# Kernel optimization log

Hardware: AMD Instinct MI355X
Metric: run time of the kernel (lower is better)

## Reference

```python
import jax, jax.numpy as jnp
import numpy as np

NEG_SLOPE = 0.2  # PyG GATv2Conv default negative_slope


def gatv2_layer(x, src, dst, edge_attr, Wl, bl, Wr, br, We, att, bias, n_nodes):
    """Faithful PyG GATv2Conv (concat=True, eval mode / no dropout).
    x: [N, Fin]; src/dst: [E]; edge_attr: [E, Fe]; att: [H, C].
    Returns [N, H*C].
    """
    H, C = att.shape
    xl = (x @ Wl + bl).reshape(-1, H, C)        # source-side transform (x_j)
    xr = (x @ Wr + br).reshape(-1, H, C)        # target-side transform (x_i)
    e_emb = (edge_attr @ We).reshape(-1, H, C)
    # per-edge pre-activation: x_i + x_j + edge
    g = jax.nn.leaky_relu(xl[src] + xr[dst] + e_emb, NEG_SLOPE)  # [E, H, C]
    logits = jnp.einsum('ehc,hc->eh', g, att)                    # [E, H]
    # segment softmax grouped by destination node
    m = jax.ops.segment_max(logits, dst, num_segments=n_nodes)   # [N, H]
    m = jnp.where(jnp.isfinite(m), m, 0.0)                       # empty segments
    a = jnp.exp(logits - m[dst])
    denom = jax.ops.segment_sum(a, dst, num_segments=n_nodes)    # [N, H]
    alpha = a / (denom[dst] + 1e-16)
    msg = xl[src] * alpha[:, :, None]                            # [E, H, C]
    out = jax.ops.segment_sum(msg, dst, num_segments=n_nodes)    # [N, H, C]
    return out.reshape(n_nodes, H * C) + bias


def setup_inputs() -> dict:
    key = jax.random.key(0)
    ks = jax.random.split(key, 24)
    N, E = 100000, 1600000
    Fin, Hd, Fe = 6, 64, 2
    g = lambda k, shp: (jax.random.normal(k, shp, dtype=jnp.float32) * 0.1)
    inp = {
        'x': jax.random.normal(ks[0], (N, Fin), dtype=jnp.float32),
        'edge_index': jax.random.randint(ks[1], (2, E), 0, N, dtype=jnp.int32),
        'edge_attr': jax.random.normal(ks[2], (E, Fe), dtype=jnp.float32),
        # layer 1: heads=2, out=64 -> H*C = 128
        'Wl1': g(ks[3], (Fin, 128)), 'bl1': jnp.zeros((128,), jnp.float32),
        'Wr1': g(ks[4], (Fin, 128)), 'br1': jnp.zeros((128,), jnp.float32),
        'We1': g(ks[5], (Fe, 128)),
        'att1': g(ks[6], (2, Hd)),
        'bias1': jnp.zeros((128,), jnp.float32),
        # layer 2: heads=1, in=128, out=64
        'Wl2': g(ks[7], (128, Hd)), 'bl2': jnp.zeros((Hd,), jnp.float32),
        'Wr2': g(ks[8], (128, Hd)), 'br2': jnp.zeros((Hd,), jnp.float32),
        'We2': g(ks[9], (Fe, Hd)),
        'att2': g(ks[10], (1, Hd)),
        'bias2': jnp.zeros((Hd,), jnp.float32),
        # MLP head
        'Wh1': g(ks[11], (Hd, Hd)), 'bh1': jnp.zeros((Hd,), jnp.float32),
        'Wh2': g(ks[12], (Hd, 1)), 'bh2': jnp.zeros((1,), jnp.float32),
    }
    return inp


def reference(x, edge_index, edge_attr,
              Wl1, bl1, Wr1, br1, We1, att1, bias1,
              Wl2, bl2, Wr2, br2, We2, att2, bias2,
              Wh1, bh1, Wh2, bh2):
    N = x.shape[0]
    src, dst = edge_index[0], edge_index[1]
    h = gatv2_layer(x, src, dst, edge_attr, Wl1, bl1, Wr1, br1, We1, att1, bias1, N)
    h = jax.nn.relu(h)
    h = gatv2_layer(h, src, dst, edge_attr, Wl2, bl2, Wr2, br2, We2, att2, bias2, N)
    h = jax.nn.relu(h)
    out = jax.nn.relu(h @ Wh1 + bh1) @ Wh2 + bh2  # [N, 1]
    return out[:, 0]
```

## Files before the change

### kernel.cpp

```cpp
#include <hip/hip_runtime.h>
#include <hip/hip_bf16.h>

#define NEG_SLOPE 0.2f
#define LOG2E 1.44269504088896f

#define NB_SHIFT 9
#define NB_NODES 512
#define NBLK_PART 256

typedef _Float16 half8 __attribute__((ext_vector_type(8)));
typedef _Float16 half4 __attribute__((ext_vector_type(4)));
typedef _Float16 half2t __attribute__((ext_vector_type(2)));
typedef float floatx2 __attribute__((ext_vector_type(2)));

__device__ __forceinline__ void ld4(float* d, const float* p) {
    float4 t = *(const float4*)p;
    d[0] = t.x; d[1] = t.y; d[2] = t.z; d[3] = t.w;
}

__device__ __forceinline__ unsigned pack2h(float a, float b) {
    union { half2t h; unsigned u; } pk;
    pk.h[0] = (_Float16)a; pk.h[1] = (_Float16)b;
    return pk.u;
}

__device__ __forceinline__ half2t u2h2(unsigned u) {
    union { unsigned u; half2t h; } c; c.u = u; return c.h;
}
__device__ __forceinline__ half2t f2h2(float a, float b) {
    half2t r; r[0] = (_Float16)a; r[1] = (_Float16)b; return r;
}

#if __has_builtin(__builtin_amdgcn_perm)
#define PERMB(a, b, s) __builtin_amdgcn_perm((a), (b), (s))
#else
__device__ __forceinline__ unsigned PERMB(unsigned a, unsigned b, unsigned s) {
    unsigned long long v = ((unsigned long long)a << 32) | b;
    unsigned r = 0;
#pragma unroll
    for (int i = 0; i < 4; ++i) {
        unsigned idx = (s >> (8 * i)) & 0xFF;
        r |= ((unsigned)(v >> (8 * idx)) & 0xFF) << (8 * i);
    }
    return r;
}
#endif

#if __has_builtin(__builtin_amdgcn_fdot2)
#define FDOT2(a, b, c) __builtin_amdgcn_fdot2((a), (b), (c), false)
#else
#define FDOT2(a, b, c) fmaf((float)(a)[1], (float)(b)[1], fmaf((float)(a)[0], (float)(b)[0], (c)))
#endif

#define DPP_ADD(x, ctrl) \
    ((x) + __int_as_float(__builtin_amdgcn_update_dpp(0, __float_as_int(x), (ctrl), 0xf, 0xf, true)))
#define ROW_REDUCE16(x) do { \
    x = DPP_ADD(x, 0x128); \
    x = DPP_ADD(x, 0x124); \
    x = DPP_ADD(x, 0x122); \
    x = DPP_ADD(x, 0x121); \
} while (0)

#define CHGRP(xl2, xr2, wa, wb, at2, ex, ey, logit) do { \
    half2t z_ = (xl2) + (xr2); \
    z_ = __builtin_elementwise_fma((ex), (wa), z_); \
    z_ = __builtin_elementwise_fma((ey), (wb), z_); \
    z_ = __builtin_elementwise_max(z_, z_ * NEGS); \
    logit = FDOT2(z_, (at2), logit); \
} while (0)

__global__ void __launch_bounds__(256) prep_kernel(
    const float* __restrict__ x,
    const float* __restrict__ Wl1, const float* __restrict__ bl1,
    const float* __restrict__ Wr1, const float* __restrict__ br1,
    _Float16* __restrict__ xlh, _Float16* __restrict__ xrh, int N)
{
    int gt = blockIdx.x * blockDim.x + threadIdx.x;
    int n = gt >> 6, c = gt & 63;
    if (n >= N) return;
    const float* xrow = x + (size_t)n * 6;
    float l0 = bl1[c], l1 = bl1[64 + c];
    float r0 = br1[c], r1 = br1[64 + c];
#pragma unroll
    for (int f = 0; f < 6; ++f) {
        float xv = xrow[f];
        l0 = fmaf(xv, Wl1[f * 128 + c], l0);
        l1 = fmaf(xv, Wl1[f * 128 + 64 + c], l1);
        r0 = fmaf(xv, Wr1[f * 128 + c], r0);
        r1 = fmaf(xv, Wr1[f * 128 + 64 + c], r1);
    }
    *(unsigned*)(xlh + (size_t)n * 128 + 2 * c) = pack2h(l0, l1);
    *(unsigned*)(xrh + (size_t)n * 128 + 2 * c) = pack2h(r0, r1);
}

__global__ void __launch_bounds__(256) partA_count(
    const int* __restrict__ dstv, int* __restrict__ M, int E, int EPB, int NB)
{
    __shared__ int hist[256];
    int blk = blockIdx.x, t = threadIdx.x;
    if (t < NB) hist[t] = 0;
    __syncthreads();
    int s0 = blk * EPB;
    int s1 = min(s0 + EPB, E);
    for (int e = s0 + t; e < s1; e += 256)
        atomicAdd(&hist[((unsigned)dstv[e]) >> NB_SHIFT], 1);
    __syncthreads();
    if (t < NB) M[t * NBLK_PART + blk] = hist[t];
}

__global__ void __launch_bounds__(256) partB1_scanrow(
    int* __restrict__ M, int* __restrict__ btot)
{
    __shared__ int lds[256];
    int bkt = blockIdx.x, t = threadIdx.x;
    int cnt = M[bkt * NBLK_PART + t];
    lds[t] = cnt;
    __syncthreads();
    for (int s = 1; s < 256; s <<= 1) {
        int v = (t >= s) ? lds[t - s] : 0;
        __syncthreads();
        lds[t] += v;
        __syncthreads();
    }
    M[bkt * NBLK_PART + t] = lds[t] - cnt;
    if (t == 255) btot[bkt] = lds[255];
}

__global__ void partB2_scanbkt(const int* __restrict__ btot, int* __restrict__ boff,
                               int* __restrict__ off, int NB, int N, int E)
{
    if (threadIdx.x == 0) {
        int run = 0;
        for (int i = 0; i < NB; ++i) { boff[i] = run; run += btot[i]; }
        boff[NB] = run;
        off[N] = E;
    }
}

__global__ void __launch_bounds__(256) partC_scatter(
    const int* __restrict__ srcv, const int* __restrict__ dstv,
    const float2* __restrict__ ea2, const int* __restrict__ M,
    const int* __restrict__ boff,
    int2* __restrict__ ebuf, int* __restrict__ dbuf,
    int E, int EPB, int NB)
{
    __shared__ int cur[256];
    int blk = blockIdx.x, t = threadIdx.x;
    if (t < NB) cur[t] = M[t * NBLK_PART + blk] + boff[t];
    __syncthreads();
    int s0 = blk * EPB;
    int s1 = min(s0 + EPB, E);
    for (int e = s0 + t; e < s1; e += 256) {
        int d = dstv[e];
        int bkt = ((unsigned)d) >> NB_SHIFT;
        int p = atomicAdd(&cur[bkt], 1);
        float2 ea = ea2[e];
        int2 v; v.x = srcv[e]; v.y = (int)pack2h(ea.x, ea.y);
        ebuf[p] = v;
        dbuf[p] = d;
    }
}

__global__ void __launch_bounds__(256) partD_finalize(
    const int2* __restrict__ ebuf, const int* __restrict__ dbuf,
    const int* __restrict__ boff,
    int* __restrict__ off, int2* __restrict__ csr_edge, int N)
{
    __shared__ int hist[NB_NODES];
    int b = blockIdx.x, t = threadIdx.x;
    int node_base = b << NB_SHIFT;
    int nnodes = min(NB_NODES, N - node_base);
    int seg_s = boff[b], seg_e = boff[b + 1];
    for (int i = t; i < NB_NODES; i += 256) hist[i] = 0;
    __syncthreads();
    for (int e = seg_s + t; e < seg_e; e += 256)
        atomicAdd(&hist[dbuf[e] - node_base], 1);
    __syncthreads();
    if (t == 0) {
        int run = 0;
        for (int i = 0; i < nnodes; ++i) { int c = hist[i]; hist[i] = run; run += c; }
    }
    __syncthreads();
    for (int i = t; i < nnodes; i += 256) off[node_base + i] = seg_s + hist[i];
    __syncthreads();
    for (int e = seg_s + t; e < seg_e; e += 256) {
        int dl = dbuf[e] - node_base;
        int r = atomicAdd(&hist[dl], 1);
        csr_edge[seg_s + r] = ebuf[e];
    }
}

__global__ void __launch_bounds__(256) c1_kernel(
    const int* __restrict__ off, const int2* __restrict__ csr_edge,
    const _Float16* __restrict__ xlh, const _Float16* __restrict__ xrh,
    const float* __restrict__ We1, const float* __restrict__ att1,
    const float* __restrict__ bias1,
    _Float16* __restrict__ h1h, int N)
{
    int wid = (blockIdx.x * blockDim.x + threadIdx.x) >> 6;
    int lane = threadIdx.x & 63;
    if (wid >= N) return;
    int n = wid;
    int g = lane & 15;
    int slot = lane >> 4;
    unsigned gb = (unsigned)(g << 4);

    const half2t NEGS = f2h2(NEG_SLOPE, NEG_SLOPE);

    half2t a0h[2], a1h[2], w00h[2], w01h[2], w10h[2], w11h[2];
    {
        float t[4];
        ld4(t, att1 + 4 * g);
        a0h[0] = f2h2(t[0] * LOG2E, t[1] * LOG2E); a0h[1] = f2h2(t[2] * LOG2E, t[3] * LOG2E);
        ld4(t, att1 + 64 + 4 * g);
        a1h[0] = f2h2(t[0] * LOG2E, t[1] * LOG2E); a1h[1] = f2h2(t[2] * LOG2E, t[3] * LOG2E);
        ld4(t, We1 + 4 * g);        w00h[0] = f2h2(t[0], t[1]); w00h[1] = f2h2(t[2], t[3]);
        ld4(t, We1 + 64 + 4 * g);   w01h[0] = f2h2(t[0], t[1]); w01h[1] = f2h2(t[2], t[3]);
        ld4(t, We1 + 128 + 4 * g);  w10h[0] = f2h2(t[0], t[1]); w10h[1] = f2h2(t[2], t[3]);
        ld4(t, We1 + 192 + 4 * g);  w11h[0] = f2h2(t[0], t[1]); w11h[1] = f2h2(t[2], t[3]);
    }

    half2t xr00, xr01, xr10, xr11;
    {
        half8 xrv = *(const half8*)(xrh + (size_t)n * 128 + 8 * g);
        xr00[0] = xrv[0]; xr00[1] = xrv[2];
        xr01[0] = xrv[4]; xr01[1] = xrv[6];
        xr10[0] = xrv[1]; xr10[1] = xrv[3];
        xr11[0] = xrv[5]; xr11[1] = xrv[7];
    }

    int s = off[n], e = off[n + 1];
    float a0A[4] = {0,0,0,0}, a1A[4] = {0,0,0,0};
    float a0B[4] = {0,0,0,0}, a1B[4] = {0,0,0,0};
    float d0A = 0.f, d1A = 0.f, d0B = 0.f, d1B = 0.f;

    const char* xlb = (const char*)xlh;

    int pA0 = s + slot, pB0 = s + 4 + slot;
    bool vA0 = (pA0 < e), vB0 = (pB0 < e);
    int2 edA0 = csr_edge[vA0 ? pA0 : s];
    int2 edB0 = csr_edge[vB0 ? pB0 : s];
    int pA1 = s + 8 + slot, pB1 = s + 12 + slot;
    bool vA1 = (pA1 < e), vB1 = (pB1 < e);
    int2 edA1 = csr_edge[vA1 ? pA1 : s];
    int2 edB1 = csr_edge[vB1 ? pB1 : s];
    half8 hvA = *(const half8*)(xlb + (((unsigned)edA0.x) << 8) + gb);
    half8 hvB = *(const half8*)(xlb + (((unsigned)edB0.x) << 8) + gb);

    for (int p0 = s; p0 < e; p0 += 8) {
        int pA2 = p0 + 16 + slot, pB2 = p0 + 20 + slot;
        bool vA2 = (pA2 < e), vB2 = (pB2 < e);
        int2 edA2 = csr_edge[vA2 ? pA2 : s];
        int2 edB2 = csr_edge[vB2 ? pB2 : s];

        half8 hvAn = *(const half8*)(xlb + (((unsigned)edA1.x) << 8) + gb);
        half8 hvBn = *(const half8*)(xlb + (((unsigned)edB1.x) << 8) + gb);

        unsigned uA = (unsigned)edA0.y, uB = (unsigned)edB0.y;
        half2t exA = u2h2(PERMB(uA, uA, 0x01000100));
        half2t eyA = u2h2(PERMB(uA, uA, 0x03020302));
        half2t exB = u2h2(PERMB(uB, uB, 0x01000100));
        half2t eyB = u2h2(PERMB(uB, uB, 0x03020302));

        union { half8 h; unsigned u[4]; } HA, HB;
        HA.h = hvA; HB.h = hvB;
        half2t xA00 = u2h2(PERMB(HA.u[1], HA.u[0], 0x05040100));
        half2t xA01 = u2h2(PERMB(HA.u[3], HA.u[2], 0x05040100));
        half2t xA10 = u2h2(PERMB(HA.u[1], HA.u[0], 0x07060302));
        half2t xA11 = u2h2(PERMB(HA.u[3], HA.u[2], 0x07060302));
        half2t xB00 = u2h2(PERMB(HB.u[1], HB.u[0], 0x05040100));
        half2t xB01 = u2h2(PERMB(HB.u[3], HB.u[2], 0x05040100));
        half2t xB10 = u2h2(PERMB(HB.u[1], HB.u[0], 0x07060302));
        half2t xB11 = u2h2(PERMB(HB.u[3], HB.u[2], 0x07060302));

        float pA0f = 0.f, pA1f = 0.f, pB0f = 0.f, pB1f = 0.f;
        CHGRP(xA00, xr00, w00h[0], w10h[0], a0h[0], exA, eyA, pA0f);
        CHGRP(xA01, xr01, w00h[1], w10h[1], a0h[1], exA, eyA, pA0f);
        CHGRP(xA10, xr10, w01h[0], w11h[0], a1h[0], exA, eyA, pA1f);
        CHGRP(xA11, xr11, w01h[1], w11h[1], a1h[1], exA, eyA, pA1f);
        CHGRP(xB00, xr00, w00h[0], w10h[0], a0h[0], exB, eyB, pB0f);
        CHGRP(xB01, xr01, w00h[1], w10h[1], a0h[1], exB, eyB, pB0f);
        CHGRP(xB10, xr10, w01h[0], w11h[0], a1h[0], exB, eyB, pB1f);
        CHGRP(xB11, xr11, w01h[1], w11h[1], a1h[1], exB, eyB, pB1f);

        ROW_REDUCE16(pA0f);
        ROW_REDUCE16(pA1f);
        ROW_REDUCE16(pB0f);
        ROW_REDUCE16(pB1f);

        float eA0 = vA0 ? exp2f(pA0f) : 0.f;
        float eA1 = vA0 ? exp2f(pA1f) : 0.f;
        float eB0 = vB0 ? exp2f(pB0f) : 0.f;
        float eB1 = vB0 ? exp2f(pB1f) : 0.f;
        d0A += eA0; d1A += eA1;
        d0B += eB0; d1B += eB1;

        a0A[0] = fmaf(eA0, (float)hvA[0], a0A[0]);
        a0A[1] = fmaf(eA0, (float)hvA[2], a0A[1]);
        a0A[2] = fmaf(eA0, (float)hvA[4], a0A[2]);
        a0A[3] = fmaf(eA0, (float)hvA[6], a0A[3]);
        a1A[0] = fmaf(eA1, (float)hvA[1], a1A[0]);
        a1A[1] = fmaf(eA1, (float)hvA[3], a1A[1]);
        a1A[2] = fmaf(eA1, (float)hvA[5], a1A[2]);
        a1A[3] = fmaf(eA1, (float)hvA[7], a1A[3]);
        a0B[0] = fmaf(eB0, (float)hvB[0], a0B[0]);
        a0B[1] = fmaf(eB0, (float)hvB[2], a0B[1]);
        a0B[2] = fmaf(eB0, (float)hvB[4], a0B[2]);
        a0B[3] = fmaf(eB0, (float)hvB[6], a0B[3]);
        a1B[0] = fmaf(eB1, (float)hvB[1], a1B[0]);
        a1B[1] = fmaf(eB1, (float)hvB[3], a1B[1]);
        a1B[2] = fmaf(eB1, (float)hvB[5], a1B[2]);
        a1B[3] = fmaf(eB1, (float)hvB[7], a1B[3]);

        edA0 = edA1; edB0 = edB1; vA0 = vA1; vB0 = vB1;
        edA1 = edA2; edB1 = edB2; vA1 = vA2; vB1 = vB2;
        hvA = hvAn; hvB = hvBn;
    }

    float acc0[4], acc1[4];
#pragma unroll
    for (int i = 0; i < 4; ++i) { acc0[i] = a0A[i] + a0B[i]; acc1[i] = a1A[i] + a1B[i]; }
    float d0 = d0A + d0B, d1 = d1A + d1B;
#pragma unroll
    for (int i = 0; i < 4; ++i) {
        acc0[i] += __shfl_xor(acc0[i], 16); acc0[i] += __shfl_xor(acc0[i], 32);
        acc1[i] += __shfl_xor(acc1[i], 16); acc1[i] += __shfl_xor(acc1[i], 32);
    }
    d0 += __shfl_xor(d0, 16); d0 += __shfl_xor(d0, 32);
    d1 += __shfl_xor(d1, 16); d1 += __shfl_xor(d1, 32);

    if (slot == 0) {
        float b0[4], b1[4];
        ld4(b0, bias1 + 4 * g);
        ld4(b1, bias1 + 64 + 4 * g);
        float r0 = 1.f / (d0 + 1e-16f), r1 = 1.f / (d1 + 1e-16f);
        half4 o0, o1;
        o0[0] = (_Float16)fmaxf(fmaf(acc0[0], r0, b0[0]), 0.f);
        o0[1] = (_Float16)fmaxf(fmaf(acc0[1], r0, b0[1]), 0.f);
        o0[2] = (_Float16)fmaxf(fmaf(acc0[2], r0, b0[2]), 0.f);
        o0[3] = (_Float16)fmaxf(fmaf(acc0[3], r0, b0[3]), 0.f);
        o1[0] = (_Float16)fmaxf(fmaf(acc1[0], r1, b1[0]), 0.f);
        o1[1] = (_Float16)fmaxf(fmaf(acc1[1], r1, b1[1]), 0.f);
        o1[2] = (_Float16)fmaxf(fmaf(acc1[2], r1, b1[2]), 0.f);
        o1[3] = (_Float16)fmaxf(fmaf(acc1[3], r1, b1[3]), 0.f);
        *(half4*)(h1h + (size_t)n * 128 + 4 * g) = o0;
        *(half4*)(h1h + (size_t)n * 128 + 64 + 4 * g) = o1;
    }
}

__global__ void __launch_bounds__(256) a2_kernel(
    const _Float16* __restrict__ h1h,
    const float* __restrict__ Wl2, const float* __restrict__ bl2,
    const float* __restrict__ Wr2, const float* __restrict__ br2,
    _Float16* __restrict__ xl2h, _Float16* __restrict__ xr2h, int N)
{
    __shared__ float hs[64 * 128];
    int tid = threadIdx.x;
    int n0 = blockIdx.x * 64;

    for (int i = tid; i < 64 * 16; i += 256) {
        int row = i >> 4;
        int q = i & 15;
        int n = n0 + row;
        float f[8];
        if (n < N) {
            half8 v = *(const half8*)(h1h + (size_t)n * 128 + q * 8);
#pragma unroll
            for (int j = 0; j < 8; ++j) f[j] = (float)v[j];
        } else {
#pragma unroll
            for (int j = 0; j < 8; ++j) f[j] = 0.f;
        }
        *(float4*)(hs + row * 128 + q * 8)     = make_float4(f[0], f[1], f[2], f[3]);
        *(float4*)(hs + row * 128 + q * 8 + 4) = make_float4(f[4], f[5], f[6], f[7]);
    }
    __syncthreads();

    int cslot = tid & 31;
    int jgrp = tid >> 5;
    int c4 = cslot * 4;
    bool isL = (c4 < 64);
    int cc = isL ? c4 : (c4 - 64);
    const float* Wb = (isL ? Wl2 : Wr2) + cc;
    const float* bb = (isL ? bl2 : br2) + cc;
    float4 bias = *(const float4*)bb;

    float acc[8][4];
#pragma unroll
    for (int j = 0; j < 8; ++j) {
        acc[j][0] = bias.x; acc[j][1] = bias.y;
        acc[j][2] = bias.z; acc[j][3] = bias.w;
    }

    const float* hrow = hs + (jgrp * 8) * 128;
#pragma unroll 2
    for (int k4 = 0; k4 < 32; ++k4) {
        float4 w0 = *(const float4*)(Wb + (4 * k4 + 0) * 64);
        float4 w1 = *(const float4*)(Wb + (4 * k4 + 1) * 64);
        float4 w2 = *(const float4*)(Wb + (4 * k4 + 2) * 64);
        float4 w3 = *(const float4*)(Wb + (4 * k4 + 3) * 64);
#pragma unroll
        for (int j = 0; j < 8; ++j) {
            float4 hv = *(const float4*)(hrow + j * 128 + k4 * 4);
            acc[j][0] = fmaf(hv.x, w0.x, acc[j][0]);
            acc[j][1] = fmaf(hv.x, w0.y, acc[j][1]);
            acc[j][2] = fmaf(hv.x, w0.z, acc[j][2]);
            acc[j][3] = fmaf(hv.x, w0.w, acc[j][3]);
            acc[j][0] = fmaf(hv.y, w1.x, acc[j][0]);
            acc[j][1] = fmaf(hv.y, w1.y, acc[j][1]);
            acc[j][2] = fmaf(hv.y, w1.z, acc[j][2]);
            acc[j][3] = fmaf(hv.y, w1.w, acc[j][3]);
            acc[j][0] = fmaf(hv.z, w2.x, acc[j][0]);
            acc[j][1] = fmaf(hv.z, w2.y, acc[j][1]);
            acc[j][2] = fmaf(hv.z, w2.z, acc[j][2]);
            acc[j][3] = fmaf(hv.z, w2.w, acc[j][3]);
            acc[j][0] = fmaf(hv.w, w3.x, acc[j][0]);
            acc[j][1] = fmaf(hv.w, w3.y, acc[j][1]);
            acc[j][2] = fmaf(hv.w, w3.z, acc[j][2]);
            acc[j][3] = fmaf(hv.w, w3.w, acc[j][3]);
        }
    }

    _Float16* outb = isL ? xl2h : xr2h;
#pragma unroll
    for (int j = 0; j < 8; ++j) {
        int n = n0 + jgrp * 8 + j;
        if (n < N) {
            half4 o;
            o[0] = (_Float16)acc[j][0];
            o[1] = (_Float16)acc[j][1];
            o[2] = (_Float16)acc[j][2];
            o[3] = (_Float16)acc[j][3];
            *(half4*)(outb + (size_t)n * 64 + cc) = o;
        }
    }
}

__global__ void __launch_bounds__(256) c2_kernel(
    const int* __restrict__ off, const int2* __restrict__ csr_edge,
    const _Float16* __restrict__ xl2h, const _Float16* __restrict__ xr2h,
    const float* __restrict__ We2, const float* __restrict__ att2,
    const float* __restrict__ bias2,
    float* __restrict__ h2out, int N)
{
    int wid = (blockIdx.x * blockDim.x + threadIdx.x) >> 6;
    int lane = threadIdx.x & 63;
    if (wid >= N) return;
    int n = wid;
    int g = lane & 15;
    int slot = lane >> 4;
    unsigned gb = (unsigned)(g << 3);

    const half2t NEGS = f2h2(NEG_SLOPE, NEG_SLOPE);

    half2t avh[2], w0h[2], w1h[2], xr2[2];
    {
        float t[4];
        ld4(t, att2 + 4 * g);
        avh[0] = f2h2(t[0] * LOG2E, t[1] * LOG2E); avh[1] = f2h2(t[2] * LOG2E, t[3] * LOG2E);
        ld4(t, We2 + 4 * g);       w0h[0] = f2h2(t[0], t[1]); w0h[1] = f2h2(t[2], t[3]);
        ld4(t, We2 + 64 + 4 * g);  w1h[0] = f2h2(t[0], t[1]); w1h[1] = f2h2(t[2], t[3]);
        half4 xh = *(const half4*)(xr2h + (size_t)n * 64 + 4 * g);
        xr2[0][0] = xh[0]; xr2[0][1] = xh[1];
        xr2[1][0] = xh[2]; xr2[1][1] = xh[3];
    }

    int s = off[n], e = off[n + 1];
    float dA = 0.f, dB = 0.f;
    float aA[4] = {0,0,0,0}, aB[4] = {0,0,0,0};

    const char* xlb = (const char*)xl2h;

    int pA0 = s + slot, pB0 = s + 4 + slot;
    bool vA0 = (pA0 < e), vB0 = (pB0 < e);
    int2 edA0 = csr_edge[vA0 ? pA0 : s];
    int2 edB0 = csr_edge[vB0 ? pB0 : s];
    int pA1 = s + 8 + slot, pB1 = s + 12 + slot;
    bool vA1 = (pA1 < e), vB1 = (pB1 < e);
    int2 edA1 = csr_edge[vA1 ? pA1 : s];
    int2 edB1 = csr_edge[vB1 ? pB1 : s];
    half4 hvA = *(const half4*)(xlb + (((unsigned)edA0.x) << 7) + gb);
    half4 hvB = *(const half4*)(xlb + (((unsigned)edB0.x) << 7) + gb);

    for (int p0 = s; p0 < e; p0 += 8) {
        int pA2 = p0 + 16 + slot, pB2 = p0 + 20 + slot;
        bool vA2 = (pA2 < e), vB2 = (pB2 < e);
        int2 edA2 = csr_edge[vA2 ? pA2 : s];
        int2 edB2 = csr_edge[vB2 ? pB2 : s];

        half4 hvAn = *(const half4*)(xlb + (((unsigned)edA1.x) << 7) + gb);
        half4 hvBn = *(const half4*)(xlb + (((unsigned)edB1.x) << 7) + gb);

        unsigned uA = (unsigned)edA0.y, uB = (unsigned)edB0.y;
        half2t exA = u2h2(PERMB(uA, uA, 0x01000100));
        half2t eyA = u2h2(PERMB(uA, uA, 0x03020302));
        half2t exB = u2h2(PERMB(uB, uB, 0x01000100));
        half2t eyB = u2h2(PERMB(uB, uB, 0x03020302));

        union { half4 h; unsigned u[2]; } HA, HB;
        HA.h = hvA; HB.h = hvB;
        half2t xA0 = u2h2(HA.u[0]), xA1 = u2h2(HA.u[1]);
        half2t xB0 = u2h2(HB.u[0]), xB1 = u2h2(HB.u[1]);

        float pA_ = 0.f, pB_ = 0.f;
        CHGRP(xA0, xr2[0], w0h[0], w1h[0], avh[0], exA, eyA, pA_);
        CHGRP(xA1, xr2[1], w0h[1], w1h[1], avh[1], exA, eyA, pA_);
        CHGRP(xB0, xr2[0], w0h[0], w1h[0], avh[0], exB, eyB, pB_);
        CHGRP(xB1, xr2[1], w0h[1], w1h[1], avh[1], exB, eyB, pB_);

        ROW_REDUCE16(pA_);
        ROW_REDUCE16(pB_);
        float evA = vA0 ? exp2f(pA_) : 0.f;
        float evB = vB0 ? exp2f(pB_) : 0.f;
        dA += evA; dB += evB;

        aA[0] = fmaf(evA, (float)hvA[0], aA[0]);
        aA[1] = fmaf(evA, (float)hvA[1], aA[1]);
        aA[2] = fmaf(evA, (float)hvA[2], aA[2]);
        aA[3] = fmaf(evA, (float)hvA[3], aA[3]);
        aB[0] = fmaf(evB, (float)hvB[0], aB[0]);
        aB[1] = fmaf(evB, (float)hvB[1], aB[1]);
        aB[2] = fmaf(evB, (float)hvB[2], aB[2]);
        aB[3] = fmaf(evB, (float)hvB[3], aB[3]);

        edA0 = edA1; edB0 = edB1; vA0 = vA1; vB0 = vB1;
        edA1 = edA2; edB1 = edB2; vA1 = vA2; vB1 = vB2;
        hvA = hvAn; hvB = hvBn;
    }

    float acc[4];
#pragma unroll
    for (int i = 0; i < 4; ++i) acc[i] = aA[i] + aB[i];
    float dsum = dA + dB;
#pragma unroll
    for (int i = 0; i < 4; ++i) {
        acc[i] += __shfl_xor(acc[i], 16);
        acc[i] += __shfl_xor(acc[i], 32);
    }
    dsum += __shfl_xor(dsum, 16);
    dsum += __shfl_xor(dsum, 32);

    if (slot == 0) {
        float b2[4];
        ld4(b2, bias2 + 4 * g);
        float r = 1.f / (dsum + 1e-16f);
        float4 o;
        o.x = fmaxf(fmaf(acc[0], r, b2[0]), 0.f);
        o.y = fmaxf(fmaf(acc[1], r, b2[1]), 0.f);
        o.z = fmaxf(fmaf(acc[2], r, b2[2]), 0.f);
        o.w = fmaxf(fmaf(acc[3], r, b2[3]), 0.f);
        *(float4*)(h2out + (size_t)n * 64 + 4 * g) = o;
    }
}

__global__ void __launch_bounds__(256) head_kernel(
    const float* __restrict__ h2, const float* __restrict__ Wh1,
    const float* __restrict__ bh1, const float* __restrict__ Wh2,
    const float* __restrict__ bh2, float* __restrict__ out, int N)
{
    __shared__ float hs[64 * 68];
    int tid = threadIdx.x;
    int n0 = blockIdx.x * 64;

    for (int i = tid; i < 64 * 16; i += 256) {
        int row = i >> 4, q = i & 15;
        int n = n0 + row;
        float4 v = (n < N) ? *(const float4*)(h2 + (size_t)n * 64 + q * 4)
                           : make_float4(0.f, 0.f, 0.f, 0.f);
        *(float4*)(hs + row * 68 + q * 4) = v;
    }
    __syncthreads();

    int cslot = tid & 15;
    int jgrp  = tid >> 4;
    int c4 = cslot * 4;
    float4 bias = *(const float4*)(bh1 + c4);

    float acc[4][4];
#pragma unroll
    for (int r = 0; r < 4; ++r) {
        acc[r][0] = bias.x; acc[r][1] = bias.y;
        acc[r][2] = bias.z; acc[r][3] = bias.w;
    }

    const float* hrow = hs + (jgrp * 4) * 68;
#pragma unroll 2
    for (int k4 = 0; k4 < 16; ++k4) {
        float4 w0 = *(const float4*)(Wh1 + (4 * k4 + 0) * 64 + c4);
        float4 w1 = *(const float4*)(Wh1 + (4 * k4 + 1) * 64 + c4);
        float4 w2 = *(const float4*)(Wh1 + (4 * k4 + 2) * 64 + c4);
        float4 w3 = *(const float4*)(Wh1 + (4 * k4 + 3) * 64 + c4);
#pragma unroll
        for (int r = 0; r < 4; ++r) {
            float4 hv = *(const float4*)(hrow + r * 68 + k4 * 4);
            acc[r][0] = fmaf(hv.x, w0.x, acc[r][0]);
            acc[r][1] = fmaf(hv.x, w0.y, acc[r][1]);
            acc[r][2] = fmaf(hv.x, w0.z, acc[r][2]);
            acc[r][3] = fmaf(hv.x, w0.w, acc[r][3]);
            acc[r][0] = fmaf(hv.y, w1.x, acc[r][0]);
            acc[r][1] = fmaf(hv.y, w1.y, acc[r][1]);
            acc[r][2] = fmaf(hv.y, w1.z, acc[r][2]);
            acc[r][3] = fmaf(hv.y, w1.w, acc[r][3]);
            acc[r][0] = fmaf(hv.z, w2.x, acc[r][0]);
            acc[r][1] = fmaf(hv.z, w2.y, acc[r][1]);
            acc[r][2] = fmaf(hv.z, w2.z, acc[r][2]);
            acc[r][3] = fmaf(hv.z, w2.w, acc[r][3]);
            acc[r][0] = fmaf(hv.w, w3.x, acc[r][0]);
            acc[r][1] = fmaf(hv.w, w3.y, acc[r][1]);
            acc[r][2] = fmaf(hv.w, w3.z, acc[r][2]);
            acc[r][3] = fmaf(hv.w, w3.w, acc[r][3]);
        }
    }

    float4 w2v = *(const float4*)(Wh2 + c4);
    float p[4];
#pragma unroll
    for (int r = 0; r < 4; ++r) {
        p[r] = fmaxf(acc[r][0], 0.f) * w2v.x
             + fmaxf(acc[r][1], 0.f) * w2v.y
             + fmaxf(acc[r][2], 0.f) * w2v.z
             + fmaxf(acc[r][3], 0.f) * w2v.w;
    }
#pragma unroll
    for (int m = 1; m <= 8; m <<= 1) {
#pragma unroll
        for (int r = 0; r < 4; ++r) p[r] += __shfl_xor(p[r], m);
    }
    if (cslot == 0) {
        float b = bh2[0];
#pragma unroll
        for (int r = 0; r < 4; ++r) {
            int n = n0 + jgrp * 4 + r;
            if (n < N) out[n] = p[r] + b;
        }
    }
}

extern "C" void kernel_launch(void* const* d_in, const int* in_sizes, int n_in,
                              void* d_out, int out_size, void* d_ws, size_t ws_size,
                              hipStream_t stream) {
    const float* x    = (const float*)d_in[0];
    const int*   ei   = (const int*)d_in[1];
    const float* ea   = (const float*)d_in[2];
    const float* Wl1  = (const float*)d_in[3];
    const float* bl1  = (const float*)d_in[4];
    const float* Wr1  = (const float*)d_in[5];
    const float* br1  = (const float*)d_in[6];
    const float* We1  = (const float*)d_in[7];
    const float* att1 = (const float*)d_in[8];
    const float* bias1= (const float*)d_in[9];
    const float* Wl2  = (const float*)d_in[10];
    const float* bl2  = (const float*)d_in[11];
    const float* Wr2  = (const float*)d_in[12];
    const float* br2  = (const float*)d_in[13];
    const float* We2  = (const float*)d_in[14];
    const float* att2 = (const float*)d_in[15];
    const float* bias2= (const float*)d_in[16];
    const float* Wh1  = (const float*)d_in[17];
    const float* bh1  = (const float*)d_in[18];
    const float* Wh2  = (const float*)d_in[19];
    const float* bh2  = (const float*)d_in[20];

    int N = in_sizes[0] / 6;
    int E = in_sizes[1] / 2;
    const int* srcv = ei;
    const int* dstv = ei + E;

    int NB = (N + NB_NODES - 1) >> NB_SHIFT;
    int EPB = (E + NBLK_PART - 1) / NBLK_PART;

    char* w = (char*)d_ws;
    auto align256 = [](size_t v) { return (v + 255) & ~(size_t)255; };
    _Float16* xlh = (_Float16*)w;
    char* ip = w + align256((size_t)N * 128 * 2);
    _Float16* xrh = (_Float16*)ip; ip += align256((size_t)N * 128 * 2);
    _Float16* h1h = (_Float16*)ip; ip += align256((size_t)N * 128 * 2);
    _Float16* xl2h = (_Float16*)ip; ip += align256((size_t)N * 64 * 2);
    _Float16* xr2h = (_Float16*)ip; ip += align256((size_t)N * 64 * 2);
    int* off = (int*)ip;  ip += align256((size_t)(N + 1) * 4);
    int* Mbuf = (int*)ip; ip += align256((size_t)NB * NBLK_PART * 4);
    int* btot = (int*)ip; ip += align256((size_t)NB * 4);
    int* boff = (int*)ip; ip += align256((size_t)(NB + 1) * 4);
    int2* csr_edge = (int2*)ip;

    int2* ebuf = (int2*)h1h;
    int* dbuf = (int*)((char*)h1h + (size_t)E * 8);

    float* h2 = (float*)xlh;

    prep_kernel<<<((size_t)N * 64 + 255) / 256, 256, 0, stream>>>(
        x, Wl1, bl1, Wr1, br1, xlh, xrh, N);
    partA_count<<<NBLK_PART, 256, 0, stream>>>(dstv, Mbuf, E, EPB, NB);
    partB1_scanrow<<<NB, 256, 0, stream>>>(Mbuf, btot);
    partB2_scanbkt<<<1, 64, 0, stream>>>(btot, boff, off, NB, N, E);
    partC_scatter<<<NBLK_PART, 256, 0, stream>>>(
        srcv, dstv, (const float2*)ea, Mbuf, boff, ebuf, dbuf, E, EPB, NB);
    partD_finalize<<<NB, 256, 0, stream>>>(ebuf, dbuf, boff, off, csr_edge, N);
    c1_kernel<<<((size_t)N * 64 + 255) / 256, 256, 0, stream>>>(
        off, csr_edge, xlh, xrh, We1, att1, bias1, h1h, N);
    a2_kernel<<<(N + 63) / 64, 256, 0, stream>>>(
        h1h, Wl2, bl2, Wr2, br2, xl2h, xr2h, N);
    c2_kernel<<<((size_t)N * 64 + 255) / 256, 256, 0, stream>>>(
        off, csr_edge, xl2h, xr2h, We2, att2, bias2, h2, N);
    head_kernel<<<(N + 63) / 64, 256, 0, stream>>>(
        h2, Wh1, bh1, Wh2, bh2, (float*)d_out, N);
}
```

Baseline: 447.7 us.

## Process two destination nodes per wavefront in GAT aggregation kernels

```diff
diff --git a/kernel.cpp b/kernel.cpp
--- a/kernel.cpp
+++ b/kernel.cpp
@@ -11,7 +11,6 @@
 typedef _Float16 half8 __attribute__((ext_vector_type(8)));
 typedef _Float16 half4 __attribute__((ext_vector_type(4)));
 typedef _Float16 half2t __attribute__((ext_vector_type(2)));
-typedef float floatx2 __attribute__((ext_vector_type(2)));
 
 __device__ __forceinline__ void ld4(float* d, const float* p) {
     float4 t = *(const float4*)p;
@@ -197,12 +196,16 @@
     const float* __restrict__ bias1,
     _Float16* __restrict__ h1h, int N)
 {
-    int wid = (blockIdx.x * blockDim.x + threadIdx.x) >> 6;
+    int wv = (blockIdx.x * blockDim.x + threadIdx.x) >> 6;
     int lane = threadIdx.x & 63;
-    if (wid >= N) return;
-    int n = wid;
-    int g = lane & 15;
-    int slot = lane >> 4;
+    if (2 * wv >= N) return;
+    int half = lane >> 5;
+    int n = 2 * wv + half;
+    bool nvalid = (n < N);
+    int nc = nvalid ? n : 0;
+    int l = lane & 31;
+    int g = l & 15;
+    int slot = (l >> 4) & 1;
     unsigned gb = (unsigned)(g << 4);
 
     const half2t NEGS = f2h2(NEG_SLOPE, NEG_SLOPE);
@@ -222,36 +225,42 @@
 
     half2t xr00, xr01, xr10, xr11;
     {
-        half8 xrv = *(const half8*)(xrh + (size_t)n * 128 + 8 * g);
+        half8 xrv = *(const half8*)(xrh + (size_t)nc * 128 + 8 * g);
         xr00[0] = xrv[0]; xr00[1] = xrv[2];
         xr01[0] = xrv[4]; xr01[1] = xrv[6];
         xr10[0] = xrv[1]; xr10[1] = xrv[3];
         xr11[0] = xrv[5]; xr11[1] = xrv[7];
     }
 
-    int s = off[n], e = off[n + 1];
+    int s = off[nc];
+    int e = nvalid ? off[nc + 1] : s;
+    int m = e - s;
+    int mo = __shfl_xor(m, 32);
+    int iters = (max(m, mo) + 3) >> 2;
+
     float a0A[4] = {0,0,0,0}, a1A[4] = {0,0,0,0};
     float a0B[4] = {0,0,0,0}, a1B[4] = {0,0,0,0};
     float d0A = 0.f, d1A = 0.f, d0B = 0.f, d1B = 0.f;
 
     const char* xlb = (const char*)xlh;
 
-    int pA0 = s + slot, pB0 = s + 4 + slot;
+    int pA0 = s + slot, pB0 = s + 2 + slot;
     bool vA0 = (pA0 < e), vB0 = (pB0 < e);
-    int2 edA0 = csr_edge[vA0 ? pA0 : s];
-    int2 edB0 = csr_edge[vB0 ? pB0 : s];
-    int pA1 = s + 8 + slot, pB1 = s + 12 + slot;
+    int2 edA0 = csr_edge[vA0 ? pA0 : 0];
+    int2 edB0 = csr_edge[vB0 ? pB0 : 0];
+    int pA1 = s + 4 + slot, pB1 = s + 6 + slot;
     bool vA1 = (pA1 < e), vB1 = (pB1 < e);
-    int2 edA1 = csr_edge[vA1 ? pA1 : s];
-    int2 edB1 = csr_edge[vB1 ? pB1 : s];
+    int2 edA1 = csr_edge[vA1 ? pA1 : 0];
+    int2 edB1 = csr_edge[vB1 ? pB1 : 0];
     half8 hvA = *(const half8*)(xlb + (((unsigned)edA0.x) << 8) + gb);
     half8 hvB = *(const half8*)(xlb + (((unsigned)edB0.x) << 8) + gb);
 
-    for (int p0 = s; p0 < e; p0 += 8) {
-        int pA2 = p0 + 16 + slot, pB2 = p0 + 20 + slot;
+    int p0 = s;
+    for (int it = 0; it < iters; ++it, p0 += 4) {
+        int pA2 = p0 + 8 + slot, pB2 = p0 + 10 + slot;
         bool vA2 = (pA2 < e), vB2 = (pB2 < e);
-        int2 edA2 = csr_edge[vA2 ? pA2 : s];
-        int2 edB2 = csr_edge[vB2 ? pB2 : s];
+        int2 edA2 = csr_edge[vA2 ? pA2 : 0];
+        int2 edB2 = csr_edge[vB2 ? pB2 : 0];
 
         half8 hvAn = *(const half8*)(xlb + (((unsigned)edA1.x) << 8) + gb);
         half8 hvBn = *(const half8*)(xlb + (((unsigned)edB1.x) << 8) + gb);
@@ -323,13 +332,13 @@
     float d0 = d0A + d0B, d1 = d1A + d1B;
 #pragma unroll
     for (int i = 0; i < 4; ++i) {
-        acc0[i] += __shfl_xor(acc0[i], 16); acc0[i] += __shfl_xor(acc0[i], 32);
-        acc1[i] += __shfl_xor(acc1[i], 16); acc1[i] += __shfl_xor(acc1[i], 32);
-    }
-    d0 += __shfl_xor(d0, 16); d0 += __shfl_xor(d0, 32);
-    d1 += __shfl_xor(d1, 16); d1 += __shfl_xor(d1, 32);
-
-    if (slot == 0) {
+        acc0[i] += __shfl_xor(acc0[i], 16);
+        acc1[i] += __shfl_xor(acc1[i], 16);
+    }
+    d0 += __shfl_xor(d0, 16);
+    d1 += __shfl_xor(d1, 16);
+
+    if (slot == 0 && nvalid) {
         float b0[4], b1[4];
         ld4(b0, bias1 + 4 * g);
         ld4(b1, bias1 + 64 + 4 * g);
@@ -443,12 +452,16 @@
     const float* __restrict__ bias2,
     float* __restrict__ h2out, int N)
 {
-    int wid = (blockIdx.x * blockDim.x + threadIdx.x) >> 6;
+    int wv = (blockIdx.x * blockDim.x + threadIdx.x) >> 6;
     int lane = threadIdx.x & 63;
-    if (wid >= N) return;
-    int n = wid;
-    int g = lane & 15;
-    int slot = lane >> 4;
+    if (2 * wv >= N) return;
+    int half = lane >> 5;
+    int n = 2 * wv + half;
+    bool nvalid = (n < N);
+    int nc = nvalid ? n : 0;
+    int l = lane & 31;
+    int g = l & 15;
+    int slot = (l >> 4) & 1;
     unsigned gb = (unsigned)(g << 3);
 
     const half2t NEGS = f2h2(NEG_SLOPE, NEG_SLOPE);
@@ -460,33 +473,39 @@
         avh[0] = f2h2(t[0] * LOG2E, t[1] * LOG2E); avh[1] = f2h2(t[2] * LOG2E, t[3] * LOG2E);
         ld4(t, We2 + 4 * g);       w0h[0] = f2h2(t[0], t[1]); w0h[1] = f2h2(t[2], t[3]);
         ld4(t, We2 + 64 + 4 * g);  w1h[0] = f2h2(t[0], t[1]); w1h[1] = f2h2(t[2], t[3]);
-        half4 xh = *(const half4*)(xr2h + (size_t)n * 64 + 4 * g);
+        half4 xh = *(const half4*)(xr2h + (size_t)nc * 64 + 4 * g);
         xr2[0][0] = xh[0]; xr2[0][1] = xh[1];
         xr2[1][0] = xh[2]; xr2[1][1] = xh[3];
     }
 
-    int s = off[n], e = off[n + 1];
+    int s = off[nc];
+    int e = nvalid ? off[nc + 1] : s;
+    int m = e - s;
+    int mo = __shfl_xor(m, 32);
+    int iters = (max(m, mo) + 3) >> 2;
+
     float dA = 0.f, dB = 0.f;
     float aA[4] = {0,0,0,0}, aB[4] = {0,0,0,0};
 
     const char* xlb = (const char*)xl2h;
 
-    int pA0 = s + slot, pB0 = s + 4 + slot;
+    int pA0 = s + slot, pB0 = s + 2 + slot;
     bool vA0 = (pA0 < e), vB0 = (pB0 < e);
-    int2 edA0 = csr_edge[vA0 ? pA0 : s];
-    int2 edB0 = csr_edge[vB0 ? pB0 : s];
-    int pA1 = s + 8 + slot, pB1 = s + 12 + slot;
+    int2 edA0 = csr_edge[vA0 ? pA0 : 0];
+    int2 edB0 = csr_edge[vB0 ? pB0 : 0];
+    int pA1 = s + 4 + slot, pB1 = s + 6 + slot;
     bool vA1 = (pA1 < e), vB1 = (pB1 < e);
-    int2 edA1 = csr_edge[vA1 ? pA1 : s];
-    int2 edB1 = csr_edge[vB1 ? pB1 : s];
+    int2 edA1 = csr_edge[vA1 ? pA1 : 0];
+    int2 edB1 = csr_edge[vB1 ? pB1 : 0];
     half4 hvA = *(const half4*)(xlb + (((unsigned)edA0.x) << 7) + gb);
     half4 hvB = *(const half4*)(xlb + (((unsigned)edB0.x) << 7) + gb);
 
-    for (int p0 = s; p0 < e; p0 += 8) {
-        int pA2 = p0 + 16 + slot, pB2 = p0 + 20 + slot;
+    int p0 = s;
+    for (int it = 0; it < iters; ++it, p0 += 4) {
+        int pA2 = p0 + 8 + slot, pB2 = p0 + 10 + slot;
         bool vA2 = (pA2 < e), vB2 = (pB2 < e);
-        int2 edA2 = csr_edge[vA2 ? pA2 : s];
-        int2 edB2 = csr_edge[vB2 ? pB2 : s];
+        int2 edA2 = csr_edge[vA2 ? pA2 : 0];
+        int2 edB2 = csr_edge[vB2 ? pB2 : 0];
 
         half4 hvAn = *(const half4*)(xlb + (((unsigned)edA1.x) << 7) + gb);
         half4 hvBn = *(const half4*)(xlb + (((unsigned)edB1.x) << 7) + gb);
@@ -533,14 +552,10 @@
     for (int i = 0; i < 4; ++i) acc[i] = aA[i] + aB[i];
     float dsum = dA + dB;
 #pragma unroll
-    for (int i = 0; i < 4; ++i) {
-        acc[i] += __shfl_xor(acc[i], 16);
-        acc[i] += __shfl_xor(acc[i], 32);
-    }
+    for (int i = 0; i < 4; ++i) acc[i] += __shfl_xor(acc[i], 16);
     dsum += __shfl_xor(dsum, 16);
-    dsum += __shfl_xor(dsum, 32);
-
-    if (slot == 0) {
+
+    if (slot == 0 && nvalid) {
         float b2[4];
         ld4(b2, bias2 + 4 * g);
         float r = 1.f / (dsum + 1e-16f);
@@ -685,7 +700,6 @@
 
     int2* ebuf = (int2*)h1h;
     int* dbuf = (int*)((char*)h1h + (size_t)E * 8);
-
     float* h2 = (float*)xlh;
 
     prep_kernel<<<((size_t)N * 64 + 255) / 256, 256, 0, stream>>>(
@@ -696,11 +710,12 @@
     partC_scatter<<<NBLK_PART, 256, 0, stream>>>(
         srcv, dstv, (const float2*)ea, Mbuf, boff, ebuf, dbuf, E, EPB, NB);
     partD_finalize<<<NB, 256, 0, stream>>>(ebuf, dbuf, boff, off, csr_edge, N);
-    c1_kernel<<<((size_t)N * 64 + 255) / 256, 256, 0, stream>>>(
+    size_t nwv = (size_t)((N + 1) / 2);
+    c1_kernel<<<(nwv * 64 + 255) / 256, 256, 0, stream>>>(
         off, csr_edge, xlh, xrh, We1, att1, bias1, h1h, N);
     a2_kernel<<<(N + 63) / 64, 256, 0, stream>>>(
         h1h, Wl2, bl2, Wr2, br2, xl2h, xr2h, N);
-    c2_kernel<<<((size_t)N * 64 + 255) / 256, 256, 0, stream>>>(
+    c2_kernel<<<(nwv * 64 + 255) / 256, 256, 0, stream>>>(
         off, csr_edge, xl2h, xr2h, We2, att2, bias2, h2, N);
     head_kernel<<<(N + 63) / 64, 256, 0, stream>>>(
         h2, Wh1, bh1, Wh2, bh2, (float*)d_out, N);
```

Measured after the change: 437.0 us. 1.02x faster.
